# Performance work log

Hardware: AMD Instinct MI355X
Metric: run time of the kernel (lower is better)

Reference implementation:

```python
import jax, jax.numpy as jnp
import numpy as np

NUM_HEADS = 8
NUM_GROUPS = 32
EPS = 1e-5
RESCALE = 1.0


def setup_inputs() -> dict:
    key = jax.random.key(0)
    ks = jax.random.split(key, 7)
    b, c, h, w = 16, 512, 32, 32
    return {
        "x": jax.random.normal(ks[0], (b, c, h, w), jnp.float32),
        "norm_w": jax.random.normal(ks[1], (c,), jnp.float32),
        "norm_b": jax.random.normal(ks[2], (c,), jnp.float32),
        "qkv_w": jax.random.normal(ks[3], (3 * c, c), jnp.float32) * (c ** -0.5),
        "qkv_b": jax.random.normal(ks[4], (3 * c,), jnp.float32) * 0.02,
        "proj_w": jax.random.normal(ks[5], (c, c), jnp.float32) * (c ** -0.5),
        "proj_b": jax.random.normal(ks[6], (c,), jnp.float32) * 0.02,
    }


def _group_norm(x, w, b):
    # x: [B, C, L]
    B, C, L = x.shape
    g = x.reshape(B, NUM_GROUPS, (C // NUM_GROUPS) * L)
    mu = jnp.mean(g, axis=-1, keepdims=True)
    var = jnp.var(g, axis=-1, keepdims=True)
    g = (g - mu) * jax.lax.rsqrt(var + EPS)
    return g.reshape(B, C, L) * w[None, :, None] + b[None, :, None]


def reference(x, norm_w, norm_b, qkv_w, qkv_b, proj_w, proj_b):
    b, c, hh, ww = x.shape
    L = hh * ww
    H = NUM_HEADS
    ch = c // H  # head dim

    xr = x.reshape(b, c, L)
    hid = _group_norm(xr, norm_w, norm_b)

    # 1x1 conv1d == matmul over channel dim: [3c, c] @ [b, c, L]
    qkv = jnp.einsum('oc,bcl->bol', qkv_w, hid) + qkv_b[None, :, None]
    # torch: reshape(b*H, 3*ch, L).split(ch) -> per-head contiguous [q|k|v] blocks
    qkv = qkv.reshape(b, H, 3, ch, L)
    q, k, v = qkv[:, :, 0], qkv[:, :, 1], qkv[:, :, 2]  # [b, H, ch, L]

    scale = 1.0 / (ch ** 0.25)
    weight = jnp.einsum('bhct,bhcs->bhts', q * scale, k * scale)
    weight = jax.nn.softmax(weight.astype(jnp.float32), axis=-1).astype(weight.dtype)
    a = jnp.einsum('bhts,bhcs->bhct', weight, v)  # [b, H, ch, L]

    h = a.reshape(b, c, L)
    h = jnp.einsum('oc,bcl->bol', proj_w, h) + proj_b[None, :, None]
    h = h.reshape(b, c, hh, ww)
    return (x + h) / RESCALE
```

## Files before the change

### kernel.cpp

```cpp
#include <hip/hip_runtime.h>
#include <hip/hip_bf16.h>
#include <stdint.h>


using f32x4  = __attribute__((ext_vector_type(4))) float;
using bf16x8 = __attribute__((ext_vector_type(8))) __bf16;
using s8v    = __attribute__((ext_vector_type(8))) short;
using s4v    = __attribute__((ext_vector_type(4))) short;

__device__ __forceinline__ short f2bf(float f){
  union { float f; unsigned u; } c; c.f = f;
  unsigned r = (c.u + 0x7FFFu + ((c.u >> 16) & 1u)) >> 16;
  return (short)r;
}

__device__ __forceinline__ float exp2_fast(float x){
#if __has_builtin(__builtin_amdgcn_exp2f)
  return __builtin_amdgcn_exp2f(x);
#else
  return exp2f(x);
#endif
}

__device__ __forceinline__ void gl_lds16(const void* g, void* l){
  __builtin_amdgcn_global_load_lds((const __attribute__((address_space(1))) void*)g,
                                   (__attribute__((address_space(3))) void*)l, 16, 0, 0);
}

__global__ void k_convw(const float* __restrict__ qw, const float* __restrict__ pw,
                        const float* __restrict__ qb,
                        short* __restrict__ qwb, short* __restrict__ pwb,
                        float* __restrict__ qbp){
  int i = blockIdx.x * 256 + threadIdx.x;
  if (i < 786432){
    int o = i >> 9, kk = i & 511;
    int h = o / 192, rem = o - h*192;
    int nr = (rem >> 6)*512 + h*64 + (rem & 63);
    qwb[nr*512 + kk] = f2bf(qw[i]);
  } else if (i < 1048576){
    int j = i - 786432;
    pwb[j] = f2bf(pw[j]);
  } else if (i < 1050112){
    int o = i - 1048576;
    int h = o / 192, rem = o - h*192;
    qbp[(rem >> 6)*512 + h*64 + (rem & 63)] = qb[o];
  }
}

__global__ __launch_bounds__(256) void k_gnorm(const float* __restrict__ x,
                                               const float* __restrict__ w,
                                               const float* __restrict__ bia,
                                               short* __restrict__ hid){
  int b = blockIdx.x >> 5;
  int g = blockIdx.x & 31;
  int tid = threadIdx.x;
  const float* xg = x + ((size_t)b*512 + g*16)*1024;
  int l0 = tid * 4;
  float v[16][4];
  float s1 = 0.f, s2 = 0.f;
  #pragma unroll
  for (int c = 0; c < 16; c++){
    f32x4 t = *(const f32x4*)(xg + c*1024 + l0);
    #pragma unroll
    for (int j = 0; j < 4; j++){ v[c][j] = t[j]; s1 += t[j]; s2 += t[j]*t[j]; }
  }
  #pragma unroll
  for (int m = 32; m; m >>= 1){ s1 += __shfl_xor(s1, m); s2 += __shfl_xor(s2, m); }
  __shared__ float r1[4], r2[4];
  int wv = tid >> 6, ln = tid & 63;
  if (ln == 0){ r1[wv] = s1; r2[wv] = s2; }
  __syncthreads();
  s1 = r1[0]+r1[1]+r1[2]+r1[3];
  s2 = r2[0]+r2[1]+r2[2]+r2[3];
  float mu = s1 * (1.f/16384.f);
  float var = s2 * (1.f/16384.f) - mu*mu;
  float rs = rsqrtf(var + 1e-5f);
  float ww[16], bb[16];
  #pragma unroll
  for (int c = 0; c < 16; c++){ ww[c] = w[g*16+c]*rs; bb[c] = bia[g*16+c]; }
  #pragma unroll
  for (int j = 0; j < 4; j++){
    short o[16];
    #pragma unroll
    for (int c = 0; c < 16; c++) o[c] = f2bf((v[c][j]-mu)*ww[c] + bb[c]);
    short* dst = hid + ((size_t)(b*1024 + l0 + j))*512 + g*16;
    *(s8v*)dst     = *(s8v*)o;
    *(s8v*)(dst+8) = *(s8v*)(o+8);
  }
}

template<int EPI>
__global__ __launch_bounds__(256) void k_gemm(
    const short* __restrict__ A, const short* __restrict__ Bm,
    const float* __restrict__ bias, const float* __restrict__ xres,
    short* __restrict__ q_t, short* __restrict__ k_t, short* __restrict__ v_t,
    float* __restrict__ outp)
{
  __shared__ short Al[2][128*64];
  __shared__ short Bl[2][128*64];
  int id = blockIdx.x;
  int xcd = id & 7, ix = id >> 3;
  int mt, nt;
  if (EPI == 0){ mt = ix % 12; nt = ix / 12; }
  else         { mt = ix & 3;  nt = ix >> 2; }
  int m0 = mt * 128;
  int n0 = (xcd + 8*nt) * 128;
  int tid = threadIdx.x;
  int lane = tid & 63;
  int wv = tid >> 6;
  int wr = wv >> 1, wc = wv & 1;
  int l15 = lane & 15, g = lane >> 4;
  f32x4 acc[4][4] = {};

  auto STAGE = [&](int db, int k0){
    #pragma unroll
    for (int i = 0; i < 8; i++){
      int cc = wv*8 + i;
      if (cc < 16){
        int slot = cc*64 + lane;
        int row = slot >> 3, off = slot & 7;
        gl_lds16(A + (size_t)(m0+row)*512 + k0 + (off ^ (row&7))*8,
                 (char*)Al[db] + cc*1024);
      } else {
        int slot = (cc-16)*64 + lane;
        int row = slot >> 3, off = slot & 7;
        gl_lds16(Bm + (size_t)(n0+row)*512 + k0 + (off ^ (row&7))*8,
                 (char*)Bl[db] + (cc-16)*1024);
      }
    }
  };

  STAGE(0, 0);
  for (int t = 0; t < 8; t++){
    if (t < 7){
      STAGE((t+1)&1, (t+1)*64);
      asm volatile("s_waitcnt vmcnt(8)" ::: "memory");
    } else {
      asm volatile("s_waitcnt vmcnt(0)" ::: "memory");
    }
    __builtin_amdgcn_s_barrier();
    int db = t & 1;
    #pragma unroll
    for (int kk = 0; kk < 2; kk++){
      bf16x8 af[4], bf[4];
      #pragma unroll
      for (int m = 0; m < 4; m++){
        int row = wr*64 + m*16 + l15;
        int byte = row*128 + (((kk*64) + (g*16)) ^ ((row&7)<<4));
        af[m] = *(const bf16x8*)((char*)Al[db] + byte);
      }
      #pragma unroll
      for (int n = 0; n < 4; n++){
        int row = wc*64 + n*16 + l15;
        int byte = row*128 + (((kk*64) + (g*16)) ^ ((row&7)<<4));
        bf[n] = *(const bf16x8*)((char*)Bl[db] + byte);
      }
      __builtin_amdgcn_s_setprio(1);
      #pragma unroll
      for (int m = 0; m < 4; m++)
        #pragma unroll
        for (int n = 0; n < 4; n++)
          acc[m][n] = __builtin_amdgcn_mfma_f32_16x16x32_bf16(af[m], bf[n], acc[m][n], 0, 0, 0);
      __builtin_amdgcn_s_setprio(0);
    }
    __builtin_amdgcn_s_barrier();
  }

  if (EPI == 0){
    int sel = m0 >> 9;
    if (sel < 2){
      const float sc = (sel == 0) ? 0.18033688011112042f : 1.0f;
      short* dstb = (sel == 0) ? q_t : k_t;
      #pragma unroll
      for (int m = 0; m < 4; m++){
        int ob = m0 + wr*64 + m*16 + (g<<2);
        int hh = (ob>>6)&7, c0 = ob&63;
        float bs[4];
        #pragma unroll
        for (int r = 0; r < 4; r++) bs[r] = bias[ob+r];
        #pragma unroll
        for (int n = 0; n < 4; n++){
          int nn = n0 + wc*64 + n*16 + l15;
          int bb = nn >> 10, ll = nn & 1023;
          int bh = bb*8 + hh;
          short o4[4];
          #pragma unroll
          for (int r = 0; r < 4; r++) o4[r] = f2bf((acc[m][n][r] + bs[r]) * sc);
          *(s4v*)(dstb + ((size_t)bh*1024 + ll)*64 + c0) = *(s4v*)o4;
        }
      }
    } else {
      short* Sc = (short*)Al;
      #pragma unroll
      for (int m = 0; m < 4; m++){
        int ob = m0 + wr*64 + m*16 + (g<<2);
        int h2 = (ob>>6)&1, cq = (ob>>4)&3;
        float bs[4];
        #pragma unroll
        for (int r = 0; r < 4; r++) bs[r] = bias[ob+r];
        #pragma unroll
        for (int n = 0; n < 4; n++){
          int nn = n0 + wc*64 + n*16 + l15;
          int sl = nn & 63, sreg = (nn>>6)&1;
          int base = (h2*2 + sreg)*4096 + ((sl>>2)*4 + cq)*64 + (sl&3);
          #pragma unroll
          for (int r = 0; r < 4; r++)
            Sc[base + (4*g + r)*4] = f2bf(acc[m][n][r] + bs[r]);
        }
      }
      __syncthreads();
      int b0  = n0 >> 10;
      int s64 = (n0 >> 6) & 15;
      int hb  = (m0 - 1024) >> 6;
      #pragma unroll
      for (int it = 0; it < 8; it++){
        int flat = it*2048 + tid*8;
        int h2 = flat >> 13, rem = flat & 8191, sreg = rem >> 12, off = rem & 4095;
        int bh = b0*8 + hb + h2;
        *(s8v*)(v_t + ((size_t)bh*16 + s64 + sreg)*4096 + off) = *(const s8v*)(Sc + flat);
      }
    }
  } else {
    #pragma unroll
    for (int m = 0; m < 4; m++){
      int ob = m0 + wr*64 + m*16 + (g<<2);
      float bs[4];
      #pragma unroll
      for (int r = 0; r < 4; r++) bs[r] = bias[ob+r];
      #pragma unroll
      for (int n = 0; n < 4; n++){
        int nn = n0 + wc*64 + n*16 + l15;
        int bb = nn >> 10, ll = nn & 1023;
        #pragma unroll
        for (int r = 0; r < 4; r++){
          size_t idx = ((size_t)bb*512 + ob + r)*1024 + ll;
          outp[idx] = xres[idx] + acc[m][n][r] + bs[r];
        }
      }
    }
  }
}

__global__ __launch_bounds__(256, 4) void k_attn(
    const short* __restrict__ q_t, const short* __restrict__ k_t,
    const short* __restrict__ v_t, short* __restrict__ a_bt)
{
  __shared__ short Kl[2][64*64];
  __shared__ short Vl[2][64*64];
  int id = blockIdx.x;
  int xcd = id & 7, ix = id >> 3;
  int bh = xcd*16 + (ix >> 3);
  int qb = ix & 7;
  int bb = bh >> 3, hh = bh & 7;
  int tid = threadIdx.x;
  int lane = tid & 63;
  int wv = tid >> 6;
  int l15 = lane & 15, g = lane >> 4;

  bf16x8 qf[2][2];
  #pragma unroll
  for (int qt = 0; qt < 2; qt++){
    const short* qbase = q_t + ((size_t)bh*1024 + qb*128 + qt*64 + wv*16 + l15)*64 + g*8;
    qf[qt][0] = *(const bf16x8*)(qbase);
    qf[qt][1] = *(const bf16x8*)(qbase + 32);
  }
  asm volatile("" :: "v"(qf[0][0]), "v"(qf[0][1]), "v"(qf[1][0]), "v"(qf[1][1]));

  bf16x8 onesb;
  #pragma unroll
  for (int i = 0; i < 8; i++) onesb[i] = (__bf16)1.0f;

  auto STAGE = [&](int db, int s0){
    #pragma unroll
    for (int i = 0; i < 4; i++){
      int cc = wv*4 + i;
      if (cc < 8){
        int slot = cc*64 + lane;
        int row = slot >> 3, off = slot & 7;
        gl_lds16(k_t + ((size_t)bh*1024 + s0 + row)*64 + (off ^ (row&7))*8,
                 (char*)Kl[db] + cc*1024);
      } else {
        gl_lds16(v_t + ((size_t)bh*16 + (s0>>6))*4096 + (cc-8)*512 + lane*8,
                 (char*)Vl[db] + (cc-8)*1024);
      }
    }
  };

  f32x4 o[2][4] = {};
  f32x4 osum[2] = {};

  STAGE(0, 0);
  for (int t = 0; t < 16; t++){
    STAGE((t+1)&1, ((t+1)&15)*64);
    asm volatile("s_waitcnt vmcnt(4)" ::: "memory");
    __builtin_amdgcn_s_barrier();
    int db = t & 1;

    f32x4 sc[2][4] = {};
    #pragma unroll
    for (int j = 0; j < 4; j++){
      #pragma unroll
      for (int ks = 0; ks < 2; ks++){
        int row = j*16 + l15;
        int byte = row*128 + (((ks*64) + (g*16)) ^ ((row&7)<<4));
        bf16x8 kf = *(const bf16x8*)((char*)Kl[db] + byte);
        __builtin_amdgcn_s_setprio(1);
        #pragma unroll
        for (int qt = 0; qt < 2; qt++)
          sc[qt][j] = __builtin_amdgcn_mfma_f32_16x16x32_bf16(kf, qf[qt][ks], sc[qt][j], 0, 0, 0);
        __builtin_amdgcn_s_setprio(0);
      }
    }

    #pragma unroll
    for (int ks = 0; ks < 2; ks++){
      bf16x8 pa[2];
      #pragma unroll
      for (int qt = 0; qt < 2; qt++){
        #pragma unroll
        for (int i2 = 0; i2 < 8; i2++)
          pa[qt][i2] = (__bf16)exp2_fast(sc[qt][2*ks + (i2>>2)][i2&3]);
        osum[qt] = __builtin_amdgcn_mfma_f32_16x16x32_bf16(pa[qt], onesb, osum[qt], 0, 0, 0);
      }
      #pragma unroll
      for (int jd = 0; jd < 4; jd++){
        union { s4v h[2]; bf16x8 b; } vb;
        vb.h[0] = *(const s4v*)((char*)Vl[db] + ks*4096        + g*512 + jd*128 + l15*8);
        vb.h[1] = *(const s4v*)((char*)Vl[db] + ks*4096 + 2048 + g*512 + jd*128 + l15*8);
        __builtin_amdgcn_s_setprio(1);
        #pragma unroll
        for (int qt = 0; qt < 2; qt++)
          o[qt][jd] = __builtin_amdgcn_mfma_f32_16x16x32_bf16(pa[qt], vb.b, o[qt][jd], 0, 0, 0);
        __builtin_amdgcn_s_setprio(0);
      }
    }
    __builtin_amdgcn_s_barrier();
  }

  #pragma unroll
  for (int qt = 0; qt < 2; qt++){
    #pragma unroll
    for (int r = 0; r < 4; r++){
      float inv = 1.f / osum[qt][r];
      int qrow = qb*128 + qt*64 + wv*16 + g*4 + r;
      #pragma unroll
      for (int jd = 0; jd < 4; jd++)
        a_bt[((size_t)bb*1024 + qrow)*512 + hh*64 + jd*16 + l15] = f2bf(o[qt][jd][r] * inv);
    }
  }
}

extern "C" void kernel_launch(void* const* d_in, const int* in_sizes, int n_in,
                              void* d_out, int out_size, void* d_ws, size_t ws_size,
                              hipStream_t stream){
  const float* x  = (const float*)d_in[0];
  const float* nw = (const float*)d_in[1];
  const float* nb = (const float*)d_in[2];
  const float* qw = (const float*)d_in[3];
  const float* qb = (const float*)d_in[4];
  const float* pw = (const float*)d_in[5];
  const float* pb = (const float*)d_in[6];
  float* outp = (float*)d_out;

  char* ws = (char*)d_ws;
  short* hid  = (short*)(ws);
  short* qwb  = (short*)(ws + 16777216);
  short* pwb  = (short*)(ws + 18350080);
  short* q_t  = (short*)(ws + 18874368);
  short* k_t  = (short*)(ws + 35651584);
  short* v_t  = (short*)(ws + 52428800);
  short* a_bt = hid;
  float* qbp  = (float*)d_out;
  if (ws_size < 69206016) return;

  k_convw<<<4103, 256, 0, stream>>>(qw, pw, qb, qwb, pwb, qbp);
  k_gnorm<<<512, 256, 0, stream>>>(x, nw, nb, hid);
  k_gemm<0><<<1536, 256, 0, stream>>>(qwb, hid, qbp, nullptr, q_t, k_t, v_t, nullptr);
  k_attn<<<1024, 256, 0, stream>>>(q_t, k_t, v_t, a_bt);
  k_gemm<1><<<512, 256, 0, stream>>>(pwb, a_bt, pb, x, nullptr, nullptr, nullptr, outp);
}
```

Measured before the change: 126.9 us.

## Restructure double-buffer sync to one barrier per tile and repack V layout

Both the QKV GEMM and the attention loop now wait for all loads, barrier once, then issue the next tile's prefetch, which drops the second barrier per iteration. The V tensor is written to the workspace in a new interleaved order so the attention kernel can fetch each V fragment with a single 16-byte LDS read instead of two 8-byte reads. K fragment loads are hoisted so both halves are read before the MFMAs. The trade-off is that the prefetch now starts after the barrier and vmcnt(0) waits for everything, which may expose more load latency.

```diff
diff --git a/kernel.cpp b/kernel.cpp
--- a/kernel.cpp
+++ b/kernel.cpp
@@ -132,13 +132,9 @@
 
   STAGE(0, 0);
   for (int t = 0; t < 8; t++){
-    if (t < 7){
-      STAGE((t+1)&1, (t+1)*64);
-      asm volatile("s_waitcnt vmcnt(8)" ::: "memory");
-    } else {
-      asm volatile("s_waitcnt vmcnt(0)" ::: "memory");
-    }
+    asm volatile("s_waitcnt vmcnt(0)" ::: "memory");
     __builtin_amdgcn_s_barrier();
+    if (t < 7) STAGE((t+1)&1, (t+1)*64);
     int db = t & 1;
     #pragma unroll
     for (int kk = 0; kk < 2; kk++){
@@ -163,8 +159,8 @@
           acc[m][n] = __builtin_amdgcn_mfma_f32_16x16x32_bf16(af[m], bf[n], acc[m][n], 0, 0, 0);
       __builtin_amdgcn_s_setprio(0);
     }
-    __builtin_amdgcn_s_barrier();
-  }
+  }
+  __builtin_amdgcn_s_barrier();
 
   if (EPI == 0){
     int sel = m0 >> 9;
@@ -202,10 +198,11 @@
         for (int n = 0; n < 4; n++){
           int nn = n0 + wc*64 + n*16 + l15;
           int sl = nn & 63, sreg = (nn>>6)&1;
-          int base = (h2*2 + sreg)*4096 + ((sl>>2)*4 + cq)*64 + (sl&3);
+          int ks2 = sl >> 5, gq = (sl>>2)&3, i2 = (sl&3) + 4*((sl>>4)&1);
+          int base = (h2*2 + sreg)*4096 + (((ks2*4+gq)*4 + cq)*16 + (g<<2))*8 + i2;
           #pragma unroll
           for (int r = 0; r < 4; r++)
-            Sc[base + (4*g + r)*4] = f2bf(acc[m][n][r] + bs[r]);
+            Sc[base + r*8] = f2bf(acc[m][n][r] + bs[r]);
         }
       }
       __syncthreads();
@@ -291,25 +288,28 @@
 
   STAGE(0, 0);
   for (int t = 0; t < 16; t++){
-    STAGE((t+1)&1, ((t+1)&15)*64);
-    asm volatile("s_waitcnt vmcnt(4)" ::: "memory");
+    asm volatile("s_waitcnt vmcnt(0)" ::: "memory");
     __builtin_amdgcn_s_barrier();
+    if (t < 15) STAGE((t+1)&1, (t+1)*64);
     int db = t & 1;
 
     f32x4 sc[2][4] = {};
     #pragma unroll
     for (int j = 0; j < 4; j++){
-      #pragma unroll
-      for (int ks = 0; ks < 2; ks++){
+      bf16x8 kf0, kf1;
+      {
         int row = j*16 + l15;
-        int byte = row*128 + (((ks*64) + (g*16)) ^ ((row&7)<<4));
-        bf16x8 kf = *(const bf16x8*)((char*)Kl[db] + byte);
-        __builtin_amdgcn_s_setprio(1);
-        #pragma unroll
-        for (int qt = 0; qt < 2; qt++)
-          sc[qt][j] = __builtin_amdgcn_mfma_f32_16x16x32_bf16(kf, qf[qt][ks], sc[qt][j], 0, 0, 0);
-        __builtin_amdgcn_s_setprio(0);
-      }
+        int swz = (row&7)<<4;
+        kf0 = *(const bf16x8*)((char*)Kl[db] + row*128 + ((g*16) ^ swz));
+        kf1 = *(const bf16x8*)((char*)Kl[db] + row*128 + ((64 + g*16) ^ swz));
+      }
+      __builtin_amdgcn_s_setprio(1);
+      #pragma unroll
+      for (int qt = 0; qt < 2; qt++){
+        sc[qt][j] = __builtin_amdgcn_mfma_f32_16x16x32_bf16(kf0, qf[qt][0], sc[qt][j], 0, 0, 0);
+        sc[qt][j] = __builtin_amdgcn_mfma_f32_16x16x32_bf16(kf1, qf[qt][1], sc[qt][j], 0, 0, 0);
+      }
+      __builtin_amdgcn_s_setprio(0);
     }
 
     #pragma unroll
@@ -324,17 +324,14 @@
       }
       #pragma unroll
       for (int jd = 0; jd < 4; jd++){
-        union { s4v h[2]; bf16x8 b; } vb;
-        vb.h[0] = *(const s4v*)((char*)Vl[db] + ks*4096        + g*512 + jd*128 + l15*8);
-        vb.h[1] = *(const s4v*)((char*)Vl[db] + ks*4096 + 2048 + g*512 + jd*128 + l15*8);
+        bf16x8 vbb = *(const bf16x8*)((char*)Vl[db] + ((ks*4+g)*4+jd)*256 + l15*16);
         __builtin_amdgcn_s_setprio(1);
         #pragma unroll
         for (int qt = 0; qt < 2; qt++)
-          o[qt][jd] = __builtin_amdgcn_mfma_f32_16x16x32_bf16(pa[qt], vb.b, o[qt][jd], 0, 0, 0);
+          o[qt][jd] = __builtin_amdgcn_mfma_f32_16x16x32_bf16(pa[qt], vbb, o[qt][jd], 0, 0, 0);
         __builtin_amdgcn_s_setprio(0);
       }
     }
-    __builtin_amdgcn_s_barrier();
   }
 
   #pragma unroll
```

Measured after the change: 123.4 us. 2.8% less time.
